# Optimization experiments

Measured on AMD Instinct MI355X. Metric: run time of the kernel, lower is better.

Reference implementation:

```python
import jax, jax.numpy as jnp
import numpy as np

B, N, D, H = 4, 2048, 512, 8
HD = D // H  # 64


def setup_inputs() -> dict:
    key = jax.random.key(0)
    ks = jax.random.split(key, 12)
    s = 0.02
    return {
        "x": jax.random.normal(ks[0], (B, N, D), jnp.float32),
        "freqs": jax.random.normal(ks[1], (B, N, HD // 2), jnp.float32),
        # weights stored as (in, out); torch Linear applies x @ W.T + b
        "wqkv_w": jax.random.normal(ks[2], (D, 3 * D), jnp.float32) * s,
        "wqkv_b": jax.random.normal(ks[3], (3 * D,), jnp.float32) * s,
        "out_w": jax.random.normal(ks[4], (D, D), jnp.float32) * s,
        "out_b": jax.random.normal(ks[5], (D,), jnp.float32) * s,
        "ffn1_w": jax.random.normal(ks[6], (2 * D, 2 * D), jnp.float32) * s,
        "ffn1_b": jax.random.normal(ks[7], (2 * D,), jnp.float32) * s,
        "ln_g": jnp.ones((2 * D,), jnp.float32),
        "ln_b": jnp.zeros((2 * D,), jnp.float32),
        "ffn2_w": jax.random.normal(ks[8], (2 * D, D), jnp.float32) * s,
        "ffn2_b": jax.random.normal(ks[9], (D,), jnp.float32) * s,
    }


def _rope(t, cos, sin):
    # t: [B,H,N,HD]; cos/sin: [B,1,N,HD/2]
    x1, x2 = t[..., ::2], t[..., 1::2]
    return jnp.stack([x1 * cos - x2 * sin, x1 * sin + x2 * cos], axis=-1).reshape(t.shape)


def reference(x, freqs, wqkv_w, wqkv_b, out_w, out_b,
              ffn1_w, ffn1_b, ln_g, ln_b, ffn2_w, ffn2_b):
    b, n, d = x.shape
    h, hd = H, d // H
    qkv = x @ wqkv_w + wqkv_b                      # [B,N,3D]
    q, k, v = jnp.split(qkv, 3, axis=-1)
    to_heads = lambda t: t.reshape(b, n, h, hd).transpose(0, 2, 1, 3)  # [B,H,N,HD]
    q, k, v = to_heads(q), to_heads(k), to_heads(v)
    cos = jnp.cos(freqs)[:, None]                  # [B,1,N,HD/2]
    sin = jnp.sin(freqs)[:, None]
    q = _rope(q, cos, sin)
    k = _rope(k, cos, sin)
    scale = hd ** -0.5
    attn = jax.nn.softmax(jnp.einsum('bhqd,bhkd->bhqk', q, k) * scale, axis=-1)
    msg = jnp.einsum('bhqk,bhkd->bhqd', attn, v).transpose(0, 2, 1, 3).reshape(b, n, d)
    msg = msg @ out_w + out_b
    # FFN on concat([x, msg]): Linear -> LayerNorm -> GELU(exact) -> Linear
    hcat = jnp.concatenate([x, msg], axis=-1) @ ffn1_w + ffn1_b   # [B,N,2D]
    mu = hcat.mean(-1, keepdims=True)
    var = hcat.var(-1, keepdims=True)
    hcat = (hcat - mu) * jax.lax.rsqrt(var + 1e-5) * ln_g + ln_b
    hcat = jax.nn.gelu(hcat, approximate=False)
    return x + hcat @ ffn2_w + ffn2_b
```

## Files before the change

kernel.cpp:

```cpp
#include <hip/hip_runtime.h>
#include <hip/hip_bf16.h>
#include <math.h>

typedef __bf16 bf16;
typedef __bf16 bf16x2 __attribute__((ext_vector_type(2)));
typedef __bf16 bf16x4 __attribute__((ext_vector_type(4)));
typedef __bf16 bf16x8 __attribute__((ext_vector_type(8)));
typedef float f32x4 __attribute__((ext_vector_type(4)));
typedef float f32x16 __attribute__((ext_vector_type(16)));

#define MFMA16(a, b, c) __builtin_amdgcn_mfma_f32_16x16x32_bf16(a, b, c, 0, 0, 0)
#define MFMA32(a, b, c) __builtin_amdgcn_mfma_f32_32x32x16_bf16(a, b, c, 0, 0, 0)


__global__ __launch_bounds__(256) void prep_kernel(
    const float* __restrict__ wqkv_w, const float* __restrict__ out_w,
    const float* __restrict__ ffn1_w, const float* __restrict__ ffn2_w,
    const float* __restrict__ x,
    const float* __restrict__ ffn1_b, const float* __restrict__ out_b,
    bf16* __restrict__ wqkv_t, bf16* __restrict__ ffn2_t,
    bf16* __restrict__ fused_t, bf16* __restrict__ ffn1bt,
    bf16* __restrict__ out_cast, bf16* __restrict__ cat,
    float* __restrict__ bias_f)
{
    const int bid = blockIdx.x, tid = threadIdx.x;
    __shared__ bf16 tile[32][33];
    __shared__ float red[256];
    if (bid >= 6656) {
        const int n = (bid - 6656) * 64 + (tid & 63);
        const int ic = tid >> 6;
        float acc = 0.f;
#pragma unroll 8
        for (int i = ic * 128; i < ic * 128 + 128; i++)
            acc += out_b[i] * ffn1_w[(size_t)(512 + i) * 1024 + n];
        red[tid] = acc;
        __syncthreads();
        if (tid < 64)
            bias_f[n] = ffn1_b[n] + red[tid] + red[tid + 64] + red[tid + 128] + red[tid + 192];
        return;
    }
    if (bid >= 2560) {
        int i = (bid - 2560) * 256 + tid;
        int row = i >> 7, col = (i & 127) << 2;
        const float4 v = *(const float4*)(&x[(size_t)row * 512 + col]);
        bf16x4 o; o[0] = (bf16)v.x; o[1] = (bf16)v.y; o[2] = (bf16)v.z; o[3] = (bf16)v.w;
        *(bf16x4*)(&cat[(size_t)row * 1024 + col]) = o;
        return;
    }
    if (bid >= 2304) {
        int i = (bid - 2304) * 1024 + tid * 4;
        const float4 v = *(const float4*)(&out_w[i]);
        bf16x4 o; o[0] = (bf16)v.x; o[1] = (bf16)v.y; o[2] = (bf16)v.z; o[3] = (bf16)v.w;
        *(bf16x4*)(&out_cast[i]) = o;
        return;
    }
    const float* src; bf16* dst; int C, ldd, bx, by;
    if (bid < 768)       { src = wqkv_w;            dst = wqkv_t;  C = 1536; ldd = 512;  int r = bid;        bx = r % 48; by = r / 48; }
    else if (bid < 1280) { src = ffn2_w;            dst = ffn2_t;  C = 512;  ldd = 1024; int r = bid - 768;  bx = r % 16; by = r / 16; }
    else if (bid < 1792) { src = ffn1_w;            dst = fused_t; C = 1024; ldd = 1024; int r = bid - 1280; bx = r % 32; by = r / 32; }
    else                 { src = ffn1_w + 512*1024; dst = ffn1bt;  C = 1024; ldd = 512;  int r = bid - 1792; bx = r % 32; by = r / 32; }
    const int tx = tid & 31, ty = tid >> 5;
    const int xx = bx * 32 + tx;
#pragma unroll
    for (int j = 0; j < 4; j++)
        tile[ty + 8 * j][tx] = (bf16)src[(size_t)(by * 32 + ty + 8 * j) * C + xx];
    __syncthreads();
    const int x2 = by * 32 + tx;
#pragma unroll
    for (int j = 0; j < 4; j++)
        dst[(size_t)(bx * 32 + ty + 8 * j) * ldd + x2] = tile[tx][ty + 8 * j];
}

__global__ __launch_bounds__(256) void rope_kernel(bf16* __restrict__ qb,
                                                   bf16* __restrict__ kb,
                                                   const float* __restrict__ freqs)
{
    const float SC = 0.125f * 1.44269504089f;
    const int bh = blockIdx.x >> 6, nblk = blockIdx.x & 63;
    const int g = threadIdx.x & 7, nl = threadIdx.x >> 3;
    const int n = nblk * 32 + nl;
    const int b = bh >> 3;
    const float4 f = *(const float4*)(&freqs[((size_t)b * 2048 + n) * 32 + g * 4]);
    float cs[4], sn[4];
    __sincosf(f.x, &sn[0], &cs[0]);
    __sincosf(f.y, &sn[1], &cs[1]);
    __sincosf(f.z, &sn[2], &cs[2]);
    __sincosf(f.w, &sn[3], &cs[3]);
    const size_t off = ((size_t)bh * 2048 + n) * 64 + g * 8;
    bf16x8 q8 = *(bf16x8*)(qb + off);
    bf16x8 k8 = *(bf16x8*)(kb + off);
#pragma unroll
    for (int i = 0; i < 4; i++) {
        float q1 = q8[2 * i], q2 = q8[2 * i + 1];
        q8[2 * i]     = (bf16)((q1 * cs[i] - q2 * sn[i]) * SC);
        q8[2 * i + 1] = (bf16)((q1 * sn[i] + q2 * cs[i]) * SC);
        float k1 = k8[2 * i], k2 = k8[2 * i + 1];
        k8[2 * i]     = (bf16)(k1 * cs[i] - k2 * sn[i]);
        k8[2 * i + 1] = (bf16)(k1 * sn[i] + k2 * cs[i]);
    }
    *(bf16x8*)(qb + off) = q8;
    *(bf16x8*)(kb + off) = k8;
}

__global__ __launch_bounds__(256) void qkv_wcomb_kernel(
    const bf16* __restrict__ cat, const bf16* __restrict__ wqkv_t,
    const float* __restrict__ wqkv_b,
    bf16* __restrict__ qbuf, bf16* __restrict__ kbuf, bf16* __restrict__ vbuf,
    const bf16* __restrict__ ffn1bt, const bf16* __restrict__ out_cast,
    bf16* __restrict__ fused_t)
{
    const int bid = blockIdx.x;
    const bool isqkv = bid < 768;
    const bf16* A; const bf16* Bt; int lda, m0, n0;
    if (isqkv) { A = cat;    lda = 1024; Bt = wqkv_t;   n0 = (bid % 12) * 128; m0 = (bid / 12) * 128; }
    else       { int r = bid - 768;
                 A = ffn1bt; lda = 512;  Bt = out_cast; n0 = (r & 3) * 128;    m0 = (r >> 2) * 128; }
    const int K = 512;

    const int tid = threadIdx.x;
    const int lane = tid & 63, wave = tid >> 6;
    const int wm = wave >> 1, wn = wave & 1;
    const int l15 = lane & 15, quad = lane >> 4;

    __shared__ bf16 As[128 * 32];
    __shared__ bf16 Bs[128 * 32];

    const int c0 = tid, c1 = tid + 256;
    const int r0 = c0 >> 2, kc0 = (c0 & 3) << 3;
    const int r1 = c1 >> 2, kc1 = (c1 & 3) << 3;
    const bf16* pA0 = &A[(size_t)(m0 + r0) * lda + kc0];
    const bf16* pA1 = &A[(size_t)(m0 + r1) * lda + kc1];
    const bf16* pB0 = &Bt[(size_t)(n0 + r0) * K + kc0];
    const bf16* pB1 = &Bt[(size_t)(n0 + r1) * K + kc1];

    const f32x4 zero = {0.f, 0.f, 0.f, 0.f};
    f32x4 acc[4][4];
#pragma unroll
    for (int i = 0; i < 4; i++)
#pragma unroll
        for (int j = 0; j < 4; j++) acc[i][j] = zero;

    bf16x8 ra0 = *(const bf16x8*)pA0;
    bf16x8 ra1 = *(const bf16x8*)pA1;
    bf16x8 rb0 = *(const bf16x8*)pB0;
    bf16x8 rb1 = *(const bf16x8*)pB1;

    for (int k0 = 0; k0 < K; k0 += 32) {
        __syncthreads();
        *(bf16x8*)(&As[c0 * 8]) = ra0;
        *(bf16x8*)(&As[c1 * 8]) = ra1;
        *(bf16x8*)(&Bs[c0 * 8]) = rb0;
        *(bf16x8*)(&Bs[c1 * 8]) = rb1;
        __syncthreads();
        if (k0 + 32 < K) {
            ra0 = *(const bf16x8*)(pA0 + k0 + 32);
            ra1 = *(const bf16x8*)(pA1 + k0 + 32);
            rb0 = *(const bf16x8*)(pB0 + k0 + 32);
            rb1 = *(const bf16x8*)(pB1 + k0 + 32);
        }
        bf16x8 af[4], bfv[4];
#pragma unroll
        for (int t = 0; t < 4; t++) {
            af[t]  = *(const bf16x8*)(&As[(wm * 64 + t * 16 + l15) * 32 + quad * 8]);
            bfv[t] = *(const bf16x8*)(&Bs[(wn * 64 + t * 16 + l15) * 32 + quad * 8]);
        }
#pragma unroll
        for (int mt = 0; mt < 4; mt++)
#pragma unroll
            for (int nt = 0; nt < 4; nt++)
                acc[mt][nt] = MFMA16(af[mt], bfv[nt], acc[mt][nt]);
    }

    const int row_base = m0 + wm * 64;
    const int col_base = n0 + wn * 64;

    if (isqkv) {
        const int sector = col_base >> 9;
        bf16* dstbase = (sector == 0) ? qbuf : (sector == 1 ? kbuf : vbuf);
#pragma unroll
        for (int nt = 0; nt < 4; nt++) {
            const int col = col_base + nt * 16 + l15;
            const int cq = col & 511;
            const int h = cq >> 6, hd = cq & 63;
            const float bv = wqkv_b[col];
#pragma unroll
            for (int mt = 0; mt < 4; mt++) {
#pragma unroll
                for (int r = 0; r < 4; r++) {
                    const int mrow = row_base + mt * 16 + quad * 4 + r;
                    const int b = mrow >> 11, n = mrow & 2047;
                    dstbase[(((size_t)b * 8 + h) * 2048 + n) * 64 + hd] =
                        (bf16)(acc[mt][nt][r] + bv);
                }
            }
        }
    } else {
#pragma unroll
        for (int nt = 0; nt < 4; nt++) {
            const int col = col_base + nt * 16 + l15;
#pragma unroll
            for (int mt = 0; mt < 4; mt++) {
#pragma unroll
                for (int r = 0; r < 4; r++) {
                    const int row = row_base + mt * 16 + quad * 4 + r;
                    fused_t[(size_t)row * 1024 + 512 + col] = (bf16)acc[mt][nt][r];
                }
            }
        }
    }
}

template <int MODE>
__global__ __launch_bounds__(256) void gemm_mfma(
    const bf16* __restrict__ A, int lda, const bf16* __restrict__ Bt,
    const float* __restrict__ bias, void* __restrict__ outv,
    const float* __restrict__ auxf, int K)
{
    const int tid = threadIdx.x;
    const int lane = tid & 63, wave = tid >> 6;
    const int wm = wave >> 1, wn = wave & 1;
    const int l15 = lane & 15, quad = lane >> 4;
    const int m0 = blockIdx.y * 128;
    const int n0 = blockIdx.x * 128;

    __shared__ bf16 As[128 * 32];
    __shared__ bf16 Bs[128 * 32];

    const int c0 = tid, c1 = tid + 256;
    const int r0 = c0 >> 2, kc0 = (c0 & 3) << 3;
    const int r1 = c1 >> 2, kc1 = (c1 & 3) << 3;
    const bf16* pA0 = &A[(size_t)(m0 + r0) * lda + kc0];
    const bf16* pA1 = &A[(size_t)(m0 + r1) * lda + kc1];
    const bf16* pB0 = &Bt[(size_t)(n0 + r0) * K + kc0];
    const bf16* pB1 = &Bt[(size_t)(n0 + r1) * K + kc1];

    const f32x4 zero = {0.f, 0.f, 0.f, 0.f};
    f32x4 acc[4][4];
#pragma unroll
    for (int i = 0; i < 4; i++)
#pragma unroll
        for (int j = 0; j < 4; j++) acc[i][j] = zero;

    bf16x8 ra0 = *(const bf16x8*)pA0;
    bf16x8 ra1 = *(const bf16x8*)pA1;
    bf16x8 rb0 = *(const bf16x8*)pB0;
    bf16x8 rb1 = *(const bf16x8*)pB1;

    for (int k0 = 0; k0 < K; k0 += 32) {
        __syncthreads();
        *(bf16x8*)(&As[c0 * 8]) = ra0;
        *(bf16x8*)(&As[c1 * 8]) = ra1;
        *(bf16x8*)(&Bs[c0 * 8]) = rb0;
        *(bf16x8*)(&Bs[c1 * 8]) = rb1;
        __syncthreads();
        if (k0 + 32 < K) {
            ra0 = *(const bf16x8*)(pA0 + k0 + 32);
            ra1 = *(const bf16x8*)(pA1 + k0 + 32);
            rb0 = *(const bf16x8*)(pB0 + k0 + 32);
            rb1 = *(const bf16x8*)(pB1 + k0 + 32);
        }
        bf16x8 af[4], bfv[4];
#pragma unroll
        for (int t = 0; t < 4; t++) {
            af[t]  = *(const bf16x8*)(&As[(wm * 64 + t * 16 + l15) * 32 + quad * 8]);
            bfv[t] = *(const bf16x8*)(&Bs[(wn * 64 + t * 16 + l15) * 32 + quad * 8]);
        }
#pragma unroll
        for (int mt = 0; mt < 4; mt++)
#pragma unroll
            for (int nt = 0; nt < 4; nt++)
                acc[mt][nt] = MFMA16(af[mt], bfv[nt], acc[mt][nt]);
    }

    const int row_base = m0 + wm * 64;
    const int col_base = n0 + wn * 64;
#pragma unroll
    for (int nt = 0; nt < 4; nt++) {
        const int col = col_base + nt * 16 + l15;
        const float bv = bias[col];
#pragma unroll
        for (int mt = 0; mt < 4; mt++) {
#pragma unroll
            for (int r = 0; r < 4; r++) {
                const int row = row_base + mt * 16 + quad * 4 + r;
                float v = acc[mt][nt][r] + bv;
                if constexpr (MODE == 2) {
                    ((bf16*)outv)[(size_t)row * 1024 + col] = (bf16)v;
                } else {
                    v += auxf[(size_t)row * 512 + col];
                    ((float*)outv)[(size_t)row * 512 + col] = v;
                }
            }
        }
    }
}

__global__ __launch_bounds__(512) void attn_kernel(const bf16* __restrict__ qb,
                                                   const bf16* __restrict__ kb,
                                                   const bf16* __restrict__ vb,
                                                   bf16* __restrict__ cat)
{
    __shared__ __align__(16) char smem[35840];
    bf16* Ks  = (bf16*)smem;
    bf16* Vts = (bf16*)(smem + 128 * 72 * 2);

    const int tid = threadIdx.x, lane = tid & 63, wave = tid >> 6;
    const int l31 = lane & 31, half = lane >> 5;
    const int qg = wave >> 2, kh = wave & 3;
    const int bh = blockIdx.x >> 5, qt = blockIdx.x & 31;
    const int b = bh >> 3, h = bh & 7;
    const size_t base = (size_t)bh * 2048 * 64;
    const int m0 = qt * 64 + qg * 32;

    bf16x8 aq[4];
#pragma unroll
    for (int k4 = 0; k4 < 4; k4++)
        aq[k4] = *(const bf16x8*)(&qb[base + (size_t)(m0 + l31) * 64 + k4 * 16 + half * 8]);

    f32x16 accO[2];
#pragma unroll
    for (int i = 0; i < 16; i++) { accO[0][i] = 0.f; accO[1][i] = 0.f; }
    float lsum = 0.f;

    int krow[2], kcol[2];
#pragma unroll
    for (int i = 0; i < 2; i++) { int c = tid + i * 512; krow[i] = c >> 3; kcol[i] = (c & 7) << 3; }
    const int vpr = tid & 63, vdg = tid >> 6;

    bf16x8 kreg[2], vr0, vr1;
    auto prefetch = [&](int key0) {
#pragma unroll
        for (int i = 0; i < 2; i++)
            kreg[i] = *(const bf16x8*)(&kb[base + (size_t)(key0 + krow[i]) * 64 + kcol[i]]);
        vr0 = *(const bf16x8*)(&vb[base + (size_t)(key0 + 2 * vpr) * 64 + vdg * 8]);
        vr1 = *(const bf16x8*)(&vb[base + (size_t)(key0 + 2 * vpr + 1) * 64 + vdg * 8]);
    };

    prefetch(0);
    const int ko = kh * 32;
    for (int kt = 0; kt < 16; kt++) {
        __syncthreads();
#pragma unroll
        for (int i = 0; i < 2; i++)
            *(bf16x8*)(&Ks[krow[i] * 72 + kcol[i]]) = kreg[i];
#pragma unroll
        for (int j = 0; j < 8; j++) {
            bf16x2 pr; pr[0] = vr0[j]; pr[1] = vr1[j];
            *(bf16x2*)(&Vts[(vdg * 8 + j) * 136 + 2 * vpr]) = pr;
        }
        __syncthreads();
        if (kt < 15) prefetch((kt + 1) * 128);

        f32x16 s;
#pragma unroll
        for (int i = 0; i < 16; i++) s[i] = 0.f;
#pragma unroll
        for (int k4 = 0; k4 < 4; k4++) {
            bf16x8 ak = *(const bf16x8*)(&Ks[(ko + l31) * 72 + k4 * 16 + half * 8]);
            s = MFMA32(ak, aq[k4], s);
        }
        float p[16];
#pragma unroll
        for (int r = 0; r < 16; r++) p[r] = __builtin_amdgcn_exp2f(s[r]);
        lsum += (((p[0] + p[1]) + (p[2] + p[3])) + ((p[4] + p[5]) + (p[6] + p[7])))
              + (((p[8] + p[9]) + (p[10] + p[11])) + ((p[12] + p[13]) + (p[14] + p[15])));
        unsigned pk[8];
#pragma unroll
        for (int i2 = 0; i2 < 8; i2++) {
            union { bf16x2 hh; unsigned u; } t;
            t.hh[0] = (bf16)p[2 * i2]; t.hh[1] = (bf16)p[2 * i2 + 1];
            pk[i2] = t.u;
        }
        const unsigned sa = half ? pk[0] : pk[2];
        const unsigned sb = half ? pk[1] : pk[3];
        const unsigned sc2 = half ? pk[4] : pk[6];
        const unsigned sd = half ? pk[5] : pk[7];
        const unsigned ra = (unsigned)__shfl_xor((int)sa, 32);
        const unsigned rb = (unsigned)__shfl_xor((int)sb, 32);
        const unsigned rc = (unsigned)__shfl_xor((int)sc2, 32);
        const unsigned rd = (unsigned)__shfl_xor((int)sd, 32);
        union { bf16x8 v; unsigned u[4]; } B0, B1;
        B0.u[0] = half ? ra : pk[0];
        B0.u[1] = half ? rb : pk[1];
        B0.u[2] = half ? pk[2] : ra;
        B0.u[3] = half ? pk[3] : rb;
        B1.u[0] = half ? rc : pk[4];
        B1.u[1] = half ? rd : pk[5];
        B1.u[2] = half ? pk[6] : rc;
        B1.u[3] = half ? pk[7] : rd;
#pragma unroll
        for (int dh = 0; dh < 2; dh++) {
            bf16x8 av0 = *(const bf16x8*)(&Vts[(dh * 32 + l31) * 136 + ko + half * 8]);
            bf16x8 av1 = *(const bf16x8*)(&Vts[(dh * 32 + l31) * 136 + ko + 16 + half * 8]);
            accO[dh] = MFMA32(av0, B0.v, accO[dh]);
            accO[dh] = MFMA32(av1, B1.v, accO[dh]);
        }
    }

    auto slotp = [&](int s) { return (float*)smem + ((s * 2 + qg) * 64 + lane) * 33; };
    __syncthreads();
    if (kh == 1 || kh == 3) {
        float* pr2 = slotp(kh >> 1);
#pragma unroll
        for (int dh = 0; dh < 2; dh++)
#pragma unroll
            for (int r = 0; r < 16; r++) pr2[dh * 16 + r] = accO[dh][r];
        pr2[32] = lsum;
    }
    __syncthreads();
    if (kh == 0 || kh == 2) {
        float* pr2 = slotp(kh >> 1);
#pragma unroll
        for (int dh = 0; dh < 2; dh++)
#pragma unroll
            for (int r = 0; r < 16; r++) accO[dh][r] += pr2[dh * 16 + r];
        lsum += pr2[32];
    }
    __syncthreads();
    if (kh == 2) {
        float* pr2 = slotp(0);
#pragma unroll
        for (int dh = 0; dh < 2; dh++)
#pragma unroll
            for (int r = 0; r < 16; r++) pr2[dh * 16 + r] = accO[dh][r];
        pr2[32] = lsum;
    }
    __syncthreads();
    if (kh == 0) {
        float* pr2 = slotp(0);
#pragma unroll
        for (int dh = 0; dh < 2; dh++)
#pragma unroll
            for (int r = 0; r < 16; r++) accO[dh][r] += pr2[dh * 16 + r];
        lsum += pr2[32];
        lsum += __shfl_xor(lsum, 32);
        const float inv = 1.0f / lsum;
        const int n = m0 + l31;
        bf16* aor = cat + ((size_t)b * 2048 + n) * 1024 + 512 + h * 64;
#pragma unroll
        for (int dh = 0; dh < 2; dh++) {
#pragma unroll
            for (int g = 0; g < 4; g++) {
                bf16x4 o4;
#pragma unroll
                for (int e = 0; e < 4; e++) o4[e] = (bf16)(accO[dh][g * 4 + e] * inv);
                *(bf16x4*)(&aor[dh * 32 + g * 8 + half * 4]) = o4;
            }
        }
    }
}

__global__ __launch_bounds__(256) void ln_gelu_kernel(bf16* __restrict__ hb,
                                                      const float* __restrict__ g,
                                                      const float* __restrict__ bt)
{
    const int row = blockIdx.x, tid = threadIdx.x;
    const int lane = tid & 63, wave = tid >> 6;
    bf16* hr = hb + (size_t)row * 1024;
    bf16x4 hv = *(const bf16x4*)(&hr[tid * 4]);
    float v0 = hv[0], v1 = hv[1], v2 = hv[2], v3 = hv[3];
    float s = v0 + v1 + v2 + v3;
    float q = v0 * v0 + v1 * v1 + v2 * v2 + v3 * v3;
    for (int o = 32; o; o >>= 1) { s += __shfl_xor(s, o); q += __shfl_xor(q, o); }
    __shared__ float red[8];
    if (lane == 0) { red[wave] = s; red[4 + wave] = q; }
    __syncthreads();
    s = red[0] + red[1] + red[2] + red[3];
    q = red[4] + red[5] + red[6] + red[7];
    const float mu = s * (1.f / 1024.f);
    const float rstd = rsqrtf(q * (1.f / 1024.f) - mu * mu + 1e-5f);
    const float4 gv = *(const float4*)(&g[tid * 4]);
    const float4 bv = *(const float4*)(&bt[tid * 4]);
    float vv[4] = {v0, v1, v2, v3};
    const float gg[4] = {gv.x, gv.y, gv.z, gv.w};
    const float bb[4] = {bv.x, bv.y, bv.z, bv.w};
    bf16x4 o4;
#pragma unroll
    for (int i = 0; i < 4; i++) {
        float y = (vv[i] - mu) * rstd * gg[i] + bb[i];
        float t = 1.5957691216f * y * (1.0f + 0.044715f * y * y);
        float e = __builtin_amdgcn_exp2f(-1.44269504089f * t);
        o4[i] = (bf16)(y * __builtin_amdgcn_rcpf(1.0f + e));
    }
    *(bf16x4*)(&hr[tid * 4]) = o4;
}

extern "C" void kernel_launch(void* const* d_in, const int* in_sizes, int n_in,
                              void* d_out, int out_size, void* d_ws, size_t ws_size,
                              hipStream_t stream) {
    (void)in_sizes; (void)n_in; (void)out_size; (void)ws_size;
    const float* x      = (const float*)d_in[0];
    const float* freqs  = (const float*)d_in[1];
    const float* wqkv_w = (const float*)d_in[2];
    const float* wqkv_b = (const float*)d_in[3];
    const float* out_w  = (const float*)d_in[4];
    const float* out_b  = (const float*)d_in[5];
    const float* ffn1_w = (const float*)d_in[6];
    const float* ffn1_b = (const float*)d_in[7];
    const float* ln_g   = (const float*)d_in[8];
    const float* ln_b   = (const float*)d_in[9];
    const float* ffn2_w = (const float*)d_in[10];
    const float* ffn2_b = (const float*)d_in[11];
    float* out = (float*)d_out;
    bf16* ws   = (bf16*)d_ws;

    bf16* wqkv_t   = ws;
    bf16* ffn2_t   = wqkv_t + 1536 * 512;
    bf16* fused_t  = ffn2_t + 512 * 1024;
    bf16* ffn1bt   = fused_t + 1024 * 1024;
    bf16* out_cast = ffn1bt + 1024 * 512;
    bf16* cat      = out_cast + 512 * 512;
    bf16* qbuf     = cat + (size_t)8192 * 1024;
    bf16* kbuf     = qbuf + (size_t)8192 * 512;
    bf16* vbuf     = kbuf + (size_t)8192 * 512;
    float* bias_f  = (float*)(vbuf + (size_t)8192 * 512);
    bf16* hbuf     = qbuf;

    prep_kernel<<<6672, 256, 0, stream>>>(wqkv_w, out_w, ffn1_w, ffn2_w, x,
                                          ffn1_b, out_b,
                                          wqkv_t, ffn2_t, fused_t, ffn1bt, out_cast, cat,
                                          bias_f);
    qkv_wcomb_kernel<<<800, 256, 0, stream>>>(cat, wqkv_t, wqkv_b, qbuf, kbuf, vbuf,
                                              ffn1bt, out_cast, fused_t);
    rope_kernel<<<2048, 256, 0, stream>>>(qbuf, kbuf, freqs);
    attn_kernel<<<1024, 512, 0, stream>>>(qbuf, kbuf, vbuf, cat);
    gemm_mfma<2><<<dim3(8, 64), 256, 0, stream>>>(cat, 1024, fused_t, bias_f, hbuf, nullptr, 1024);
    ln_gelu_kernel<<<8192, 256, 0, stream>>>(hbuf, ln_g, ln_b);
    gemm_mfma<3><<<dim3(4, 64), 256, 0, stream>>>(hbuf, 1024, ffn2_t, ffn2_b, out, x, 1024);
}
```

Before: 253.5 us.

## Fuse RoPE into QKV GEMM epilogue and read K fragments directly from global

Precomputes a packed bf16 cos/sin table in the prep kernel, then applies RoPE (plus the Q scale) inside the QKV GEMM epilogue using a lane shuffle to fetch the pair element. This removes the separate rope kernel and its extra read/write pass over Q and K. The attention kernel also stops staging K through shared memory and loads K MFMA fragments straight from global memory, which removes one LDS store and read per tile but relies on cache hits for the now less-coalesced global loads. The cos/sin values are now rounded to bf16, which slightly reduces precision.

```diff
diff --git a/kernel.cpp b/kernel.cpp
--- a/kernel.cpp
+++ b/kernel.cpp
@@ -16,16 +16,31 @@
 __global__ __launch_bounds__(256) void prep_kernel(
     const float* __restrict__ wqkv_w, const float* __restrict__ out_w,
     const float* __restrict__ ffn1_w, const float* __restrict__ ffn2_w,
-    const float* __restrict__ x,
+    const float* __restrict__ x, const float* __restrict__ freqs,
     const float* __restrict__ ffn1_b, const float* __restrict__ out_b,
     bf16* __restrict__ wqkv_t, bf16* __restrict__ ffn2_t,
     bf16* __restrict__ fused_t, bf16* __restrict__ ffn1bt,
     bf16* __restrict__ out_cast, bf16* __restrict__ cat,
-    float* __restrict__ bias_f)
+    float* __restrict__ bias_f, unsigned* __restrict__ tab)
 {
     const int bid = blockIdx.x, tid = threadIdx.x;
     __shared__ bf16 tile[32][33];
     __shared__ float red[256];
+    if (bid >= 6672) {
+        int i = (bid - 6672) * 1024 + tid * 4;
+        const float4 f = *(const float4*)(&freqs[i]);
+        float s0, c0, s1, c1, s2, c2, s3, c3;
+        __sincosf(f.x, &s0, &c0); __sincosf(f.y, &s1, &c1);
+        __sincosf(f.z, &s2, &c2); __sincosf(f.w, &s3, &c3);
+        union { bf16x2 h2; unsigned u; } p0, p1, p2, p3;
+        p0.h2[0] = (bf16)c0; p0.h2[1] = (bf16)s0;
+        p1.h2[0] = (bf16)c1; p1.h2[1] = (bf16)s1;
+        p2.h2[0] = (bf16)c2; p2.h2[1] = (bf16)s2;
+        p3.h2[0] = (bf16)c3; p3.h2[1] = (bf16)s3;
+        uint4 o = {p0.u, p1.u, p2.u, p3.u};
+        *(uint4*)(&tab[i]) = o;
+        return;
+    }
     if (bid >= 6656) {
         const int n = (bid - 6656) * 64 + (tid & 63);
         const int ic = tid >> 6;
@@ -71,40 +86,9 @@
         dst[(size_t)(bx * 32 + ty + 8 * j) * ldd + x2] = tile[tx][ty + 8 * j];
 }
 
-__global__ __launch_bounds__(256) void rope_kernel(bf16* __restrict__ qb,
-                                                   bf16* __restrict__ kb,
-                                                   const float* __restrict__ freqs)
-{
-    const float SC = 0.125f * 1.44269504089f;
-    const int bh = blockIdx.x >> 6, nblk = blockIdx.x & 63;
-    const int g = threadIdx.x & 7, nl = threadIdx.x >> 3;
-    const int n = nblk * 32 + nl;
-    const int b = bh >> 3;
-    const float4 f = *(const float4*)(&freqs[((size_t)b * 2048 + n) * 32 + g * 4]);
-    float cs[4], sn[4];
-    __sincosf(f.x, &sn[0], &cs[0]);
-    __sincosf(f.y, &sn[1], &cs[1]);
-    __sincosf(f.z, &sn[2], &cs[2]);
-    __sincosf(f.w, &sn[3], &cs[3]);
-    const size_t off = ((size_t)bh * 2048 + n) * 64 + g * 8;
-    bf16x8 q8 = *(bf16x8*)(qb + off);
-    bf16x8 k8 = *(bf16x8*)(kb + off);
-#pragma unroll
-    for (int i = 0; i < 4; i++) {
-        float q1 = q8[2 * i], q2 = q8[2 * i + 1];
-        q8[2 * i]     = (bf16)((q1 * cs[i] - q2 * sn[i]) * SC);
-        q8[2 * i + 1] = (bf16)((q1 * sn[i] + q2 * cs[i]) * SC);
-        float k1 = k8[2 * i], k2 = k8[2 * i + 1];
-        k8[2 * i]     = (bf16)(k1 * cs[i] - k2 * sn[i]);
-        k8[2 * i + 1] = (bf16)(k1 * sn[i] + k2 * cs[i]);
-    }
-    *(bf16x8*)(qb + off) = q8;
-    *(bf16x8*)(kb + off) = k8;
-}
-
 __global__ __launch_bounds__(256) void qkv_wcomb_kernel(
     const bf16* __restrict__ cat, const bf16* __restrict__ wqkv_t,
-    const float* __restrict__ wqkv_b,
+    const float* __restrict__ wqkv_b, const unsigned* __restrict__ tab,
     bf16* __restrict__ qbuf, bf16* __restrict__ kbuf, bf16* __restrict__ vbuf,
     const bf16* __restrict__ ffn1bt, const bf16* __restrict__ out_cast,
     bf16* __restrict__ fused_t)
@@ -122,8 +106,10 @@
     const int wm = wave >> 1, wn = wave & 1;
     const int l15 = lane & 15, quad = lane >> 4;
 
-    __shared__ bf16 As[128 * 32];
-    __shared__ bf16 Bs[128 * 32];
+    __shared__ __align__(16) char smem[16384];
+    bf16* As = (bf16*)smem;
+    bf16* Bs = (bf16*)(smem + 8192);
+    unsigned* tabs = (unsigned*)smem;
 
     const int c0 = tid, c1 = tid + 256;
     const int r0 = c0 >> 2, kc0 = (c0 & 3) << 3;
@@ -176,6 +162,17 @@
 
     if (isqkv) {
         const int sector = col_base >> 9;
+        const bool dorope = sector < 2;
+        if (dorope) {
+            __syncthreads();
+#pragma unroll
+            for (int ps = 0; ps < 4; ps++) {
+                int idx = ps * 1024 + tid * 4;
+                *(uint4*)(&tabs[idx]) = *(const uint4*)(&tab[(size_t)m0 * 32 + idx]);
+            }
+            __syncthreads();
+        }
+        const float SCQ = 0.125f * 1.44269504089f;
         bf16* dstbase = (sector == 0) ? qbuf : (sector == 1 ? kbuf : vbuf);
 #pragma unroll
         for (int nt = 0; nt < 4; nt++) {
@@ -183,14 +180,26 @@
             const int cq = col & 511;
             const int h = cq >> 6, hd = cq & 63;
             const float bv = wqkv_b[col];
+            const int ihalf = hd >> 1;
+            const bool odd = (hd & 1) != 0;
 #pragma unroll
             for (int mt = 0; mt < 4; mt++) {
 #pragma unroll
                 for (int r = 0; r < 4; r++) {
                     const int mrow = row_base + mt * 16 + quad * 4 + r;
+                    float v = acc[mt][nt][r] + bv;
+                    float o = v;
+                    if (dorope) {
+                        float p = __shfl_xor(v, 1);
+                        const int rl = wm * 64 + mt * 16 + quad * 4 + r;
+                        union { unsigned u; bf16x2 h2; } t2;
+                        t2.u = tabs[rl * 32 + ihalf];
+                        float cs = t2.h2[0], sn = t2.h2[1];
+                        o = odd ? (p * sn + v * cs) : (v * cs - p * sn);
+                        if (sector == 0) o *= SCQ;
+                    }
                     const int b = mrow >> 11, n = mrow & 2047;
-                    dstbase[(((size_t)b * 8 + h) * 2048 + n) * 64 + hd] =
-                        (bf16)(acc[mt][nt][r] + bv);
+                    dstbase[(((size_t)b * 8 + h) * 2048 + n) * 64 + hd] = (bf16)o;
                 }
             }
         }
@@ -300,9 +309,8 @@
                                                    const bf16* __restrict__ vb,
                                                    bf16* __restrict__ cat)
 {
-    __shared__ __align__(16) char smem[35840];
-    bf16* Ks  = (bf16*)smem;
-    bf16* Vts = (bf16*)(smem + 128 * 72 * 2);
+    __shared__ __align__(16) char smem[33792];
+    bf16* Vts = (bf16*)smem;
 
     const int tid = threadIdx.x, lane = tid & 63, wave = tid >> 6;
     const int l31 = lane & 31, half = lane >> 5;
@@ -322,43 +330,38 @@
     for (int i = 0; i < 16; i++) { accO[0][i] = 0.f; accO[1][i] = 0.f; }
     float lsum = 0.f;
 
-    int krow[2], kcol[2];
-#pragma unroll
-    for (int i = 0; i < 2; i++) { int c = tid + i * 512; krow[i] = c >> 3; kcol[i] = (c & 7) << 3; }
     const int vpr = tid & 63, vdg = tid >> 6;
-
-    bf16x8 kreg[2], vr0, vr1;
-    auto prefetch = [&](int key0) {
-#pragma unroll
-        for (int i = 0; i < 2; i++)
-            kreg[i] = *(const bf16x8*)(&kb[base + (size_t)(key0 + krow[i]) * 64 + kcol[i]]);
+    bf16x8 vr0, vr1;
+    auto prefetchV = [&](int key0) {
         vr0 = *(const bf16x8*)(&vb[base + (size_t)(key0 + 2 * vpr) * 64 + vdg * 8]);
         vr1 = *(const bf16x8*)(&vb[base + (size_t)(key0 + 2 * vpr + 1) * 64 + vdg * 8]);
     };
 
-    prefetch(0);
+    prefetchV(0);
     const int ko = kh * 32;
+    const bf16* kfbase = kb + base + (size_t)(ko + l31) * 64 + half * 8;
     for (int kt = 0; kt < 16; kt++) {
-        __syncthreads();
-#pragma unroll
-        for (int i = 0; i < 2; i++)
-            *(bf16x8*)(&Ks[krow[i] * 72 + kcol[i]]) = kreg[i];
+        const int key0 = kt * 128;
+        __syncthreads();
 #pragma unroll
         for (int j = 0; j < 8; j++) {
             bf16x2 pr; pr[0] = vr0[j]; pr[1] = vr1[j];
             *(bf16x2*)(&Vts[(vdg * 8 + j) * 136 + 2 * vpr]) = pr;
         }
         __syncthreads();
-        if (kt < 15) prefetch((kt + 1) * 128);
+        if (kt < 15) prefetchV((kt + 1) * 128);
+
+        bf16x8 akf[4];
+        const bf16* kf = kfbase + (size_t)key0 * 64;
+#pragma unroll
+        for (int k4 = 0; k4 < 4; k4++) akf[k4] = *(const bf16x8*)(kf + k4 * 16);
 
         f32x16 s;
 #pragma unroll
         for (int i = 0; i < 16; i++) s[i] = 0.f;
 #pragma unroll
-        for (int k4 = 0; k4 < 4; k4++) {
-            bf16x8 ak = *(const bf16x8*)(&Ks[(ko + l31) * 72 + k4 * 16 + half * 8]);
-            s = MFMA32(ak, aq[k4], s);
-        }
+        for (int k4 = 0; k4 < 4; k4++) s = MFMA32(akf[k4], aq[k4], s);
+
         float p[16];
 #pragma unroll
         for (int r = 0; r < 16; r++) p[r] = __builtin_amdgcn_exp2f(s[r]);
@@ -514,15 +517,15 @@
     bf16* kbuf     = qbuf + (size_t)8192 * 512;
     bf16* vbuf     = kbuf + (size_t)8192 * 512;
     float* bias_f  = (float*)(vbuf + (size_t)8192 * 512);
+    unsigned* tab  = (unsigned*)(bias_f + 1024);
     bf16* hbuf     = qbuf;
 
-    prep_kernel<<<6672, 256, 0, stream>>>(wqkv_w, out_w, ffn1_w, ffn2_w, x,
+    prep_kernel<<<6928, 256, 0, stream>>>(wqkv_w, out_w, ffn1_w, ffn2_w, x, freqs,
                                           ffn1_b, out_b,
                                           wqkv_t, ffn2_t, fused_t, ffn1bt, out_cast, cat,
-                                          bias_f);
-    qkv_wcomb_kernel<<<800, 256, 0, stream>>>(cat, wqkv_t, wqkv_b, qbuf, kbuf, vbuf,
+                                          bias_f, tab);
+    qkv_wcomb_kernel<<<800, 256, 0, stream>>>(cat, wqkv_t, wqkv_b, tab, qbuf, kbuf, vbuf,
                                               ffn1bt, out_cast, fused_t);
-    rope_kernel<<<2048, 256, 0, stream>>>(qbuf, kbuf, freqs);
     attn_kernel<<<1024, 512, 0, stream>>>(qbuf, kbuf, vbuf, cat);
     gemm_mfma<2><<<dim3(8, 64), 256, 0, stream>>>(cat, 1024, fused_t, bias_f, hbuf, nullptr, 1024);
     ln_gelu_kernel<<<8192, 256, 0, stream>>>(hbuf, ln_g, ln_b);
```

Measured after the change: 299.4 us. 18.1% more time.
